# Kernel tuning notes

Hardware: AMD Instinct MI355X
Metric: run time of the kernel (lower is better)

## Reference

```python
import jax, jax.numpy as jnp
import numpy as np

DIM = 1024
HEADS = 16
HEAD_DIM = DIM // HEADS
RPE_K = 16
B, T = 4, 1024


def setup_inputs() -> dict:
    key = jax.random.key(0)
    ks = jax.random.split(key, 12)
    s = 1.0 / np.sqrt(DIM)
    inp = {
        'q': jax.random.normal(ks[0], (B, T, DIM), jnp.float32),
        'k': jax.random.normal(ks[1], (B, T, DIM), jnp.float32),
        'v': jax.random.normal(ks[2], (B, T, DIM), jnp.float32),
        'Wq': jax.random.normal(ks[3], (DIM, DIM), jnp.float32) * s,
        'bq': jnp.zeros((DIM,), jnp.float32),
        'Wk': jax.random.normal(ks[4], (DIM, DIM), jnp.float32) * s,
        'bk': jnp.zeros((DIM,), jnp.float32),
        'Wv': jax.random.normal(ks[5], (DIM, DIM), jnp.float32) * s,
        'bv': jnp.zeros((DIM,), jnp.float32),
        'rpe_w': jax.random.normal(ks[6], (2 * RPE_K + 1, 2 * HEAD_DIM), jnp.float32) * 0.02,
        'Wo': jax.random.normal(ks[7], (DIM, DIM), jnp.float32) * s,
        'bo': jnp.zeros((DIM,), jnp.float32),
    }
    return inp


def reference(q, k, v, Wq, bq, Wk, bk, Wv, bv, rpe_w, Wo, bo):
    b, ql = q.shape[:2]
    kl = k.shape[1]
    split = lambda x: x.reshape(b, -1, HEADS, HEAD_DIM).transpose(0, 2, 1, 3)  # b h t d
    qh = split(q @ Wq.T + bq)
    kh = split(k @ Wk.T + bk)
    vh = split(v @ Wv.T + bv)
    # note: original scales q BEFORE both the k-dot and the rpe_q einsum
    qh = qh / np.sqrt(HEAD_DIM)
    # relative distance table (constant ints)
    idx = jnp.arange(max(ql, kl))
    dist = jnp.clip(idx[:, None] - idx[None, :], -RPE_K, RPE_K) + RPE_K
    dist = dist[:ql, :kl]
    rpe = rpe_w[dist]                      # (ql, kl, 2*HEAD_DIM)
    rpe_q, rpe_v = jnp.split(rpe, 2, axis=-1)
    energy = jnp.einsum('bhqd,bhkd->bhqk', qh, kh)
    energy = energy + jnp.einsum('bhqd,qkd->bhqk', qh, rpe_q)
    alignment = jax.nn.softmax(energy, axis=-1)
    context = jnp.einsum('bhqk,bhkd->bhqd', alignment, vh)
    context = context + jnp.einsum('bhqk,qkd->bhqd', alignment, rpe_v)
    context = context.transpose(0, 2, 1, 3).reshape(b, ql, DIM)
    out = context @ Wo.T + bo
    return (out, alignment)
```

## Files before the change

kernel.cpp:

```cpp
#include <hip/hip_runtime.h>
#include <stdint.h>

typedef unsigned short u16;
typedef unsigned int   u32;
typedef short bf16x8 __attribute__((ext_vector_type(8)));
typedef float floatx4 __attribute__((ext_vector_type(4)));

#define OFF_XQ   0u
#define OFF_XK   4194304u
#define OFF_XV   8388608u
#define OFF_WQ   12582912u
#define OFF_WK   13631488u
#define OFF_WV   14680064u
#define OFF_WO   15728640u
#define OFF_QH   16777216u
#define OFF_KH   20971520u
#define OFF_VT   25165824u
#define OFF_CTX  29360128u

__device__ __forceinline__ u16 f2b(float f){
  u32 u = __float_as_uint(f);
  u = (u + 0x7fffu + ((u >> 16) & 1u)) >> 16;
  return (u16)u;
}
__device__ __forceinline__ float b2f(u16 h){
  return __uint_as_float(((u32)h) << 16);
}

__global__ __launch_bounds__(256) void convert_kernel(
    const float* __restrict__ q, const float* __restrict__ k, const float* __restrict__ v,
    const float* __restrict__ Wq, const float* __restrict__ Wk, const float* __restrict__ Wv,
    const float* __restrict__ Wo, u16* __restrict__ ws){
  int y = blockIdx.y;
  const float* src; u16* dst; int n;
  switch(y){
    case 0: src=q;  dst=ws+OFF_XQ; n=4194304; break;
    case 1: src=k;  dst=ws+OFF_XK; n=4194304; break;
    case 2: src=v;  dst=ws+OFF_XV; n=4194304; break;
    case 3: src=Wq; dst=ws+OFF_WQ; n=1048576; break;
    case 4: src=Wk; dst=ws+OFF_WK; n=1048576; break;
    case 5: src=Wv; dst=ws+OFF_WV; n=1048576; break;
    default:src=Wo; dst=ws+OFF_WO; n=1048576; break;
  }
  int idx = (blockIdx.x*256 + threadIdx.x)*4;
  if (idx >= n) return;
  float4 f = *(const float4*)(src + idx);
  ushort4 o;
  o.x = f2b(f.x); o.y = f2b(f.y); o.z = f2b(f.z); o.w = f2b(f.w);
  *(ushort4*)(dst + idx) = o;
}

template<int MODE>
__global__ __launch_bounds__(256) void gemm_kernel(
    const u16* __restrict__ A0, const u16* __restrict__ B0,
    const float* __restrict__ b0, const float* __restrict__ b1, const float* __restrict__ b2,
    u16* __restrict__ ws, float* __restrict__ outF){
  __shared__ u16 As[128][40];
  __shared__ u16 Bs[128][40];
  int z = (MODE==0) ? blockIdx.z : 0;
  const u16* A  = A0 + (size_t)z*4194304u;
  const u16* Bm = B0 + (size_t)z*1048576u;
  const float* bias = (MODE==0) ? (z==0?b0:(z==1?b1:b2)) : b0;
  int tid  = threadIdx.x;
  int lane = tid & 63, wave = tid >> 6;
  int wm = (wave>>1)*64, wn = (wave&1)*64;
  int m_base = blockIdx.y*128, n_base = blockIdx.x*128;
  floatx4 acc[4][4] = {};
  int fr = lane & 15, fo = (lane>>4)*8;
  for (int kb = 0; kb < 1024; kb += 32){
    #pragma unroll
    for (int p=0;p<2;p++){
      int L = tid + p*256;
      int row = L>>2, seg = (L&3)*8;
      *(uint4*)(&As[row][seg]) = *(const uint4*)(A  + (size_t)(m_base+row)*1024 + kb + seg);
      *(uint4*)(&Bs[row][seg]) = *(const uint4*)(Bm + (size_t)(n_base+row)*1024 + kb + seg);
    }
    __syncthreads();
    bf16x8 af[4], bfr[4];
    #pragma unroll
    for (int i=0;i<4;i++){
      af[i]  = *(const bf16x8*)(&As[wm + i*16 + fr][fo]);
      bfr[i] = *(const bf16x8*)(&Bs[wn + i*16 + fr][fo]);
    }
    #pragma unroll
    for (int i=0;i<4;i++)
      #pragma unroll
      for (int j=0;j<4;j++)
        acc[i][j] = __builtin_amdgcn_mfma_f32_16x16x32_bf16(af[i], bfr[j], acc[i][j], 0,0,0);
    __syncthreads();
  }
  int col = lane & 15, rb = (lane>>4)*4;
  #pragma unroll
  for (int i=0;i<4;i++){
    #pragma unroll
    for (int j=0;j<4;j++){
      int nn = n_base + wn + j*16 + col;
      float bv = bias[nn];
      #pragma unroll
      for (int r=0;r<4;r++){
        int mm = m_base + wm + i*16 + rb + r;
        float v = acc[i][j][r] + bv;
        if (MODE==0){
          if (z==0) v *= 0.125f;
          int b = mm>>10, t = mm&1023, h = nn>>6, d = nn&63;
          u32 base = (z==0)?OFF_QH:((z==1)?OFF_KH:OFF_VT);
          u32 idx = ((u32)(b*16+h))<<16;
          idx += (z==2) ? ((u32)(d<<10)+(u32)t) : ((u32)(t<<6)+(u32)d);
          ws[base + idx] = f2b(v);
        } else {
          outF[(size_t)mm*1024 + nn] = v;
        }
      }
    }
  }
}

__global__ __launch_bounds__(256) void attn_kernel(
    const u16* __restrict__ ws, const float* __restrict__ rpe_w,
    float* __restrict__ d_out, u16* __restrict__ ctx){
  __shared__ u16   P[16][1032];
  __shared__ u16   qs[16][64];
  __shared__ float proj[16][33];
  __shared__ float rpev[33][64];
  __shared__ float sacc[16][3];
  __shared__ float slds[16][33];
  __shared__ float linv[16];

  int bid = blockIdx.x;
  int qt = bid & 63, bh = bid >> 6;
  int q0 = qt * 16;
  int tid = threadIdx.x, lane = tid & 63, wave = tid >> 6;

  const u16* qh = ws + OFF_QH + (size_t)bh*65536;
  const u16* kh = ws + OFF_KH + (size_t)bh*65536;
  const u16* vT = ws + OFF_VT + (size_t)bh*65536;

  if (tid < 128){
    int r = tid >> 3, c = (tid & 7)*8;
    *(uint4*)(&qs[r][c]) = *(const uint4*)(qh + (size_t)(q0+r)*64 + c);
  }
  for (int i = tid; i < 33*64; i += 256){
    int t = i >> 6, d = i & 63;
    rpev[t][d] = rpe_w[t*128 + 64 + d];
  }
  if (tid < 48) ((float*)sacc)[tid] = 0.f;
  __syncthreads();

  for (int i = tid; i < 16*33; i += 256){
    int r = i / 33, t = i - r*33;
    float s = 0.f;
    #pragma unroll
    for (int d=0; d<64; d++) s += b2f(qs[r][d]) * rpe_w[t*128 + d];
    proj[r][t] = s;
  }
  __syncthreads();

  int col = lane & 15, rb = (lane>>4)*4, fo = (lane>>4)*8;
  bf16x8 aq0 = *(const bf16x8*)(&qs[col][fo]);
  bf16x8 aq1 = *(const bf16x8*)(&qs[col][32 + fo]);

  float tot[4] = {0,0,0,0}, lo[4] = {0,0,0,0}, hi[4] = {0,0,0,0};
  for (int kb = 0; kb < 1024; kb += 64){
    int key = kb + wave*16 + col;
    const u16* kp = kh + (size_t)key*64 + fo;
    bf16x8 bk0 = *(const bf16x8*)(kp);
    bf16x8 bk1 = *(const bf16x8*)(kp + 32);
    floatx4 s4 = {0.f,0.f,0.f,0.f};
    s4 = __builtin_amdgcn_mfma_f32_16x16x32_bf16(aq0, bk0, s4, 0,0,0);
    s4 = __builtin_amdgcn_mfma_f32_16x16x32_bf16(aq1, bk1, s4, 0,0,0);
    #pragma unroll
    for (int r=0;r<4;r++){
      int row = rb + r;
      int qg = q0 + row;
      int dd = qg - key;
      int bkt = min(max(dd, -16), 16) + 16;
      float p = __expf(s4[r] + proj[row][bkt]);
      P[row][key] = f2b(p);
      tot[r] += p;
      if      (key <= qg - 16) lo[r] += p;
      else if (key >= qg + 16) hi[r] += p;
    }
  }
  #pragma unroll
  for (int r=0;r<4;r++){
    #pragma unroll
    for (int m=8;m>=1;m>>=1){
      tot[r] += __shfl_xor(tot[r], m, 16);
      lo[r]  += __shfl_xor(lo[r],  m, 16);
      hi[r]  += __shfl_xor(hi[r],  m, 16);
    }
  }
  if (col == 0){
    #pragma unroll
    for (int r=0;r<4;r++){
      atomicAdd(&sacc[rb+r][0], tot[r]);
      atomicAdd(&sacc[rb+r][1], lo[r]);
      atomicAdd(&sacc[rb+r][2], hi[r]);
    }
  }
  __syncthreads();

  if (tid < 16){
    linv[tid] = 1.f / sacc[tid][0];
    slds[tid][32] = sacc[tid][1];
    slds[tid][0]  = sacc[tid][2];
  }
  for (int i = tid; i < 16*31; i += 256){
    int r = i / 31, t = 1 + (i - r*31);
    int kk = q0 + r + 16 - t;
    slds[r][t] = (kk >= 0 && kk < 1024) ? b2f(P[r][kk]) : 0.f;
  }
  __syncthreads();

  {
    int row = tid >> 4, c0 = (tid & 15)*4;
    float li = linv[row];
    float* outA = d_out + 4194304u + ((size_t)(bh*1024 + q0 + row))*1024;
    #pragma unroll
    for (int i=0;i<16;i++){
      int kcol = c0 + i*64;
      ushort4 pv = *(const ushort4*)(&P[row][kcol]);
      float4 o;
      o.x = b2f(pv.x)*li; o.y = b2f(pv.y)*li;
      o.z = b2f(pv.z)*li; o.w = b2f(pv.w)*li;
      *(float4*)(outA + kcol) = o;
    }
  }

  floatx4 o4 = {0.f,0.f,0.f,0.f};
  int n0 = wave*16;
  {
    const u16* vbase = vT + (size_t)(n0 + col)*1024;
    for (int kk = 0; kk < 1024; kk += 32){
      bf16x8 ap  = *(const bf16x8*)(&P[col][kk + fo]);
      bf16x8 bv8 = *(const bf16x8*)(vbase + kk + fo);
      o4 = __builtin_amdgcn_mfma_f32_16x16x32_bf16(ap, bv8, o4, 0,0,0);
    }
  }
  {
    int b = bh >> 4, h = bh & 15;
    #pragma unroll
    for (int r=0;r<4;r++){
      int row = rb + r;
      int d = n0 + col;
      float sv = 0.f;
      #pragma unroll
      for (int t=0;t<33;t++) sv += slds[row][t]*rpev[t][d];
      float v = (o4[r] + sv) * linv[row];
      ctx[((size_t)(b*1024 + q0 + row))*1024 + h*64 + d] = f2b(v);
    }
  }
}

extern "C" void kernel_launch(void* const* d_in, const int* in_sizes, int n_in,
                              void* d_out, int out_size, void* d_ws, size_t ws_size,
                              hipStream_t stream){
  const float* q  = (const float*)d_in[0];
  const float* k  = (const float*)d_in[1];
  const float* v  = (const float*)d_in[2];
  const float* Wq = (const float*)d_in[3];
  const float* bq = (const float*)d_in[4];
  const float* Wk = (const float*)d_in[5];
  const float* bk = (const float*)d_in[6];
  const float* Wv = (const float*)d_in[7];
  const float* bv = (const float*)d_in[8];
  const float* rpe= (const float*)d_in[9];
  const float* Wo = (const float*)d_in[10];
  const float* bo = (const float*)d_in[11];
  u16* ws = (u16*)d_ws;
  float* out = (float*)d_out;

  convert_kernel<<<dim3(4096,7), 256, 0, stream>>>(q,k,v,Wq,Wk,Wv,Wo, ws);
  gemm_kernel<0><<<dim3(8,32,3), 256, 0, stream>>>(ws+OFF_XQ, ws+OFF_WQ, bq, bk, bv, ws, nullptr);
  attn_kernel<<<dim3(4096), 256, 0, stream>>>(ws, rpe, out, ws+OFF_CTX);
  gemm_kernel<1><<<dim3(8,32), 256, 0, stream>>>(ws+OFF_CTX, ws+OFF_WO, bo, nullptr, nullptr, ws, out);
}
```

Measured before the change: 604.0 us.

## Use direct global-to-LDS loads in GEMM, split V projection, retile output GEMM

The GEMM now stages A and B tiles with global_load_lds direct-to-LDS copies and drops the padded shared arrays. The V projection gets its own transposed-GEMM mode (weights as A, activations as B), so the V-transpose stores are coalesced along t. The output projection uses 64-wide N tiles for more blocks. The attention kernel no longer stages rpe_v in LDS and reads it from global inside a loop reordered across rows. Removing the LDS padding risks bank conflicts, and the global rpe reads may add latency.

Result: faster. 579.1 us (-4.1%).

```diff
diff --git a/kernel.cpp b/kernel.cpp
--- a/kernel.cpp
+++ b/kernel.cpp
@@ -55,37 +55,53 @@
     const u16* __restrict__ A0, const u16* __restrict__ B0,
     const float* __restrict__ b0, const float* __restrict__ b1, const float* __restrict__ b2,
     u16* __restrict__ ws, float* __restrict__ outF){
-  __shared__ u16 As[128][40];
-  __shared__ u16 Bs[128][40];
+  constexpr int BN = (MODE==0) ? 128 : 64;
+  constexpr int NJ = BN/32;
+  __shared__ u16 As[128][32];
+  __shared__ u16 Bs[BN][32];
   int z = (MODE==0) ? blockIdx.z : 0;
   const u16* A  = A0 + (size_t)z*4194304u;
   const u16* Bm = B0 + (size_t)z*1048576u;
-  const float* bias = (MODE==0) ? (z==0?b0:(z==1?b1:b2)) : b0;
+  const float* bias = (MODE==0) ? (z==0?b0:b1) : b0;
   int tid  = threadIdx.x;
   int lane = tid & 63, wave = tid >> 6;
-  int wm = (wave>>1)*64, wn = (wave&1)*64;
-  int m_base = blockIdx.y*128, n_base = blockIdx.x*128;
-  floatx4 acc[4][4] = {};
+  int wm = (wave>>1)*64, wn = (wave&1)*(BN/2);
+  int m_base = blockIdx.y*128, n_base = blockIdx.x*BN;
+  floatx4 acc[4][NJ] = {};
   int fr = lane & 15, fo = (lane>>4)*8;
+  int srow = lane >> 2, sseg = (lane & 3)*8;
+  u16* AsW0 = &As[wave*32][0];
+  u16* AsW1 = &As[wave*32+16][0];
+  const u16* Ag0 = A  + (size_t)(m_base + wave*32      + srow)*1024 + sseg;
+  const u16* Ag1 = A  + (size_t)(m_base + wave*32 + 16 + srow)*1024 + sseg;
+  u16* BsW0; u16* BsW1; const u16* Bg0; const u16* Bg1;
+  if constexpr (BN==128){
+    BsW0 = &Bs[wave*32][0];    BsW1 = &Bs[wave*32+16][0];
+    Bg0 = Bm + (size_t)(n_base + wave*32      + srow)*1024 + sseg;
+    Bg1 = Bm + (size_t)(n_base + wave*32 + 16 + srow)*1024 + sseg;
+  } else {
+    BsW0 = &Bs[wave*16][0];    BsW1 = nullptr;
+    Bg0 = Bm + (size_t)(n_base + wave*16 + srow)*1024 + sseg;
+    Bg1 = nullptr;
+  }
   for (int kb = 0; kb < 1024; kb += 32){
-    #pragma unroll
-    for (int p=0;p<2;p++){
-      int L = tid + p*256;
-      int row = L>>2, seg = (L&3)*8;
-      *(uint4*)(&As[row][seg]) = *(const uint4*)(A  + (size_t)(m_base+row)*1024 + kb + seg);
-      *(uint4*)(&Bs[row][seg]) = *(const uint4*)(Bm + (size_t)(n_base+row)*1024 + kb + seg);
-    }
+    __builtin_amdgcn_global_load_lds((const u32*)(Ag0 + kb), (u32*)AsW0, 16, 0, 0);
+    __builtin_amdgcn_global_load_lds((const u32*)(Ag1 + kb), (u32*)AsW1, 16, 0, 0);
+    __builtin_amdgcn_global_load_lds((const u32*)(Bg0 + kb), (u32*)BsW0, 16, 0, 0);
+    if constexpr (BN==128)
+      __builtin_amdgcn_global_load_lds((const u32*)(Bg1 + kb), (u32*)BsW1, 16, 0, 0);
     __syncthreads();
-    bf16x8 af[4], bfr[4];
-    #pragma unroll
-    for (int i=0;i<4;i++){
+    bf16x8 af[4], bfr[NJ];
+    #pragma unroll
+    for (int i=0;i<4;i++)
       af[i]  = *(const bf16x8*)(&As[wm + i*16 + fr][fo]);
-      bfr[i] = *(const bf16x8*)(&Bs[wn + i*16 + fr][fo]);
-    }
+    #pragma unroll
+    for (int j=0;j<NJ;j++)
+      bfr[j] = *(const bf16x8*)(&Bs[wn + j*16 + fr][fo]);
     #pragma unroll
     for (int i=0;i<4;i++)
       #pragma unroll
-      for (int j=0;j<4;j++)
+      for (int j=0;j<NJ;j++)
         acc[i][j] = __builtin_amdgcn_mfma_f32_16x16x32_bf16(af[i], bfr[j], acc[i][j], 0,0,0);
     __syncthreads();
   }
@@ -93,22 +109,26 @@
   #pragma unroll
   for (int i=0;i<4;i++){
     #pragma unroll
-    for (int j=0;j<4;j++){
+    for (int j=0;j<NJ;j++){
       int nn = n_base + wn + j*16 + col;
-      float bv = bias[nn];
+      float bvn = (MODE==2) ? 0.f : bias[nn];
       #pragma unroll
       for (int r=0;r<4;r++){
         int mm = m_base + wm + i*16 + rb + r;
-        float v = acc[i][j][r] + bv;
-        if (MODE==0){
+        if constexpr (MODE==0){
+          float v = acc[i][j][r] + bvn;
           if (z==0) v *= 0.125f;
           int b = mm>>10, t = mm&1023, h = nn>>6, d = nn&63;
-          u32 base = (z==0)?OFF_QH:((z==1)?OFF_KH:OFF_VT);
-          u32 idx = ((u32)(b*16+h))<<16;
-          idx += (z==2) ? ((u32)(d<<10)+(u32)t) : ((u32)(t<<6)+(u32)d);
+          u32 base = (z==0)?OFF_QH:OFF_KH;
+          u32 idx = (((u32)(b*16+h))<<16) + ((u32)(t<<6)) + (u32)d;
           ws[base + idx] = f2b(v);
+        } else if constexpr (MODE==1){
+          outF[(size_t)mm*1024 + nn] = acc[i][j][r] + bvn;
         } else {
-          outF[(size_t)mm*1024 + nn] = v;
+          float v = acc[i][j][r] + bias[mm];
+          int h = mm>>6, d = mm&63, b = nn>>10, t = nn&1023;
+          u32 idx = (((u32)(b*16+h))<<16) + ((u32)(d<<10)) + (u32)t;
+          ws[OFF_VT + idx] = f2b(v);
         }
       }
     }
@@ -121,7 +141,6 @@
   __shared__ u16   P[16][1032];
   __shared__ u16   qs[16][64];
   __shared__ float proj[16][33];
-  __shared__ float rpev[33][64];
   __shared__ float sacc[16][3];
   __shared__ float slds[16][33];
   __shared__ float linv[16];
@@ -138,10 +157,6 @@
   if (tid < 128){
     int r = tid >> 3, c = (tid & 7)*8;
     *(uint4*)(&qs[r][c]) = *(const uint4*)(qh + (size_t)(q0+r)*64 + c);
-  }
-  for (int i = tid; i < 33*64; i += 256){
-    int t = i >> 6, d = i & 63;
-    rpev[t][d] = rpe_w[t*128 + 64 + d];
   }
   if (tid < 48) ((float*)sacc)[tid] = 0.f;
   __syncthreads();
@@ -239,14 +254,19 @@
   }
   {
     int b = bh >> 4, h = bh & 15;
+    int d = n0 + col;
+    float sv[4] = {0.f,0.f,0.f,0.f};
+    const float* rv = rpe_w + 64 + d;
+    #pragma unroll
+    for (int t=0;t<33;t++){
+      float rvt = rv[t*128];
+      #pragma unroll
+      for (int r=0;r<4;r++) sv[r] += slds[rb+r][t]*rvt;
+    }
     #pragma unroll
     for (int r=0;r<4;r++){
       int row = rb + r;
-      int d = n0 + col;
-      float sv = 0.f;
-      #pragma unroll
-      for (int t=0;t<33;t++) sv += slds[row][t]*rpev[t][d];
-      float v = (o4[r] + sv) * linv[row];
+      float v = (o4[r] + sv[r]) * linv[row];
       ctx[((size_t)(b*1024 + q0 + row))*1024 + h*64 + d] = f2b(v);
     }
   }
@@ -271,7 +291,8 @@
   float* out = (float*)d_out;
 
   convert_kernel<<<dim3(4096,7), 256, 0, stream>>>(q,k,v,Wq,Wk,Wv,Wo, ws);
-  gemm_kernel<0><<<dim3(8,32,3), 256, 0, stream>>>(ws+OFF_XQ, ws+OFF_WQ, bq, bk, bv, ws, nullptr);
+  gemm_kernel<0><<<dim3(8,32,2), 256, 0, stream>>>(ws+OFF_XQ, ws+OFF_WQ, bq, bk, nullptr, ws, nullptr);
+  gemm_kernel<2><<<dim3(64,8),   256, 0, stream>>>(ws+OFF_WV, ws+OFF_XV, bv, nullptr, nullptr, ws, nullptr);
   attn_kernel<<<dim3(4096), 256, 0, stream>>>(ws, rpe, out, ws+OFF_CTX);
-  gemm_kernel<1><<<dim3(8,32), 256, 0, stream>>>(ws+OFF_CTX, ws+OFF_WO, bo, nullptr, nullptr, ws, out);
-}
+  gemm_kernel<1><<<dim3(16,32), 256, 0, stream>>>(ws+OFF_CTX, ws+OFF_WO, bo, nullptr, nullptr, ws, out);
+}
```
